# Kernel optimization log

Measured on AMD Instinct MI355X. Metric: run time of the kernel, lower is better.

The kernel has to match this reference:

```python
import jax, jax.numpy as jnp
import numpy as np

B, S, D = 4, 4096, 768

def setup_inputs() -> dict:
    key = jax.random.key(0)
    kx, kq, kk, kv = jax.random.split(key, 4)
    x = jax.random.normal(kx, (B, S, D), dtype=jnp.float32)
    Wq = jax.random.normal(kq, (D, D), dtype=jnp.float32) * (D ** -0.5)
    Wk = jax.random.normal(kk, (D, D), dtype=jnp.float32) * (D ** -0.5)
    Wv = jax.random.normal(kv, (D, D), dtype=jnp.float32) * (D ** -0.5)
    return {"x": x, "Wq": Wq, "Wk": Wk, "Wv": Wv}

def reference(x, Wq, Wk, Wv):
    # q,k,v: [B,S,D]  (Linear with no bias)
    q = x @ Wq
    k = x @ Wk
    v = x @ Wv
    # full N x N causal score matrix, as in the original module
    scores = jnp.einsum('bqd,bkd->bqk', q, k)  # [B,S,S]
    seq = scores.shape[1]
    causal_mask = jnp.triu(jnp.ones((seq, seq), dtype=bool), k=1)  # True above diagonal
    scores = jnp.where(causal_mask[None, :, :], -jnp.inf, scores)
    scale = jnp.asarray(k.shape[-1], scores.dtype) ** 0.5
    weights = jax.nn.softmax(scores / scale, axis=-1)  # [B,S,S]
    # dropout p=0.0 -> identity (deterministic reference)
    context = jnp.einsum('bqk,bkd->bqd', weights, v)  # [B,S,D]
    return context
```

## Files before the change

### kernel.cpp

```cpp
#include <hip/hip_runtime.h>
#include <hip/hip_bf16.h>

typedef __attribute__((ext_vector_type(8))) _Float16 half8_t;
typedef __attribute__((ext_vector_type(4))) _Float16 half4_t;
typedef __attribute__((ext_vector_type(4))) float float4_t;

#define D_DIM 768
#define S_DIM 4096
#define B_DIM 4
#define M_DIM (B_DIM * S_DIM)
#define SD ((size_t)S_DIM * D_DIM)

#define GLOAD_LDS16(g, s)                                      \
  __builtin_amdgcn_global_load_lds(                            \
      (const __attribute__((address_space(1))) void*)(g),      \
      (__attribute__((address_space(3))) void*)(s), 16, 0, 0)

__device__ __forceinline__ float4_t mfma16(half8_t a, half8_t b, float4_t c) {
  return __builtin_amdgcn_mfma_f32_16x16x32_f16(a, b, c, 0, 0, 0);
}

__global__ __launch_bounds__(256) void cvt_x_kernel(const float* __restrict__ in,
                                                    _Float16* __restrict__ out, int n) {
  int i = (blockIdx.x * 256 + threadIdx.x) * 4;
  if (i < n) {
    float4 v = *(const float4*)(in + i);
    half4_t o;
    o.x = (_Float16)v.x; o.y = (_Float16)v.y; o.z = (_Float16)v.z; o.w = (_Float16)v.w;
    *(half4_t*)(out + i) = o;
  }
}

__global__ __launch_bounds__(256) void transpose_w_kernel(const float* __restrict__ W0,
                                                          const float* __restrict__ W1,
                                                          const float* __restrict__ W2,
                                                          _Float16* __restrict__ WT) {
  const float* W = (blockIdx.z == 0) ? W0 : (blockIdx.z == 1) ? W1 : W2;
  _Float16* o = WT + (size_t)blockIdx.z * D_DIM * D_DIM;
  __shared__ _Float16 tile[64][68];
  int k0 = blockIdx.x * 64, n0 = blockIdx.y * 64;
#pragma unroll
  for (int i = 0; i < 16; ++i) {
    int idx = threadIdx.x + i * 256;
    int r = idx >> 6, c = idx & 63;
    tile[r][c] = (_Float16)W[(size_t)(k0 + r) * D_DIM + n0 + c];
  }
  __syncthreads();
#pragma unroll
  for (int i = 0; i < 16; ++i) {
    int idx = threadIdx.x + i * 256;
    int r = idx >> 6, c = idx & 63;
    o[(size_t)(n0 + r) * D_DIM + k0 + c] = tile[c][r];
  }
}

template <int NWC, int MF, int NF, int BN, bool SWAP>
__device__ __forceinline__ void gemm_core8(const _Float16* __restrict__ Ag,
                                           const _Float16* __restrict__ Bg,
                                           int lda, int ldb, int k0t, int nt,
                                           char* AshP, char* BshP,
                                           float4_t (&acc)[MF][NF]) {
  constexpr int BR = BN / 64;
  constexpr int ASZ = 256 * 128;
  constexpr int BSZ = BN * 128;
  const int tid = threadIdx.x;
  const int w = tid >> 6, l = tid & 63;
  const int wr = w / NWC, wc = w % NWC;
  const int l15 = l & 15, l4 = l >> 4;

  int sArow[4], sAu[4], sAdst[4];
#pragma unroll
  for (int i = 0; i < 4; ++i) {
    int L = i * 512 + tid;
    int row = L >> 3;
    sArow[i] = row;
    sAu[i] = ((L & 7) ^ (row & 7)) * 8;
    sAdst[i] = (i * 512 + (tid & ~63)) * 16;
  }
  int sBrow[BR], sBu[BR], sBdst[BR];
#pragma unroll
  for (int i = 0; i < BR; ++i) {
    int L = i * 512 + tid;
    int row = L >> 3;
    sBrow[i] = row;
    sBu[i] = ((L & 7) ^ (row & 7)) * 8;
    sBdst[i] = (i * 512 + (tid & ~63)) * 16;
  }

#define STAGE8(kt, s)                                                          \
  do {                                                                         \
    _Pragma("unroll") for (int i = 0; i < 4; ++i)                              \
        GLOAD_LDS16(Ag + (size_t)sArow[i] * lda + (kt)*64 + sAu[i],            \
                    AshP + (size_t)(s)*ASZ + sAdst[i]);                        \
    _Pragma("unroll") for (int i = 0; i < BR; ++i)                             \
        GLOAD_LDS16(Bg + (size_t)sBrow[i] * ldb + (kt)*64 + sBu[i],            \
                    BshP + (size_t)(s)*BSZ + sBdst[i]);                        \
  } while (0)

  STAGE8(k0t, 0);
  for (int t = 0; t < nt; ++t) {
    const int s = t & 1;
    const char* As = AshP + (size_t)s * ASZ;
    const char* Bs = BshP + (size_t)s * BSZ;
    asm volatile("s_waitcnt vmcnt(0)" ::: "memory");
    __builtin_amdgcn_s_barrier();
    __builtin_amdgcn_sched_barrier(0);
    if (t + 1 < nt) STAGE8(k0t + t + 1, s ^ 1);
    half8_t bf[NF][2];
#pragma unroll
    for (int ni = 0; ni < NF; ++ni) {
      int brow = wc * (NF * 16) + ni * 16 + l15;
      int bb = brow * 128 + ((l4 ^ (brow & 7)) * 16);
      bf[ni][0] = *(const half8_t*)(Bs + bb);
      bf[ni][1] = *(const half8_t*)(Bs + (bb ^ 64));
    }
    __builtin_amdgcn_s_setprio(1);
#pragma unroll
    for (int mq = 0; mq < MF / 4; ++mq) {
      half8_t af[4][2];
#pragma unroll
      for (int mi = 0; mi < 4; ++mi) {
        int arow = wr * (MF * 16) + (mq * 4 + mi) * 16 + l15;
        int ab = arow * 128 + ((l4 ^ (arow & 7)) * 16);
        af[mi][0] = *(const half8_t*)(As + ab);
        af[mi][1] = *(const half8_t*)(As + (ab ^ 64));
      }
#pragma unroll
      for (int mi = 0; mi < 4; ++mi)
#pragma unroll
        for (int ni = 0; ni < NF; ++ni) {
          if (SWAP) {
            acc[mq * 4 + mi][ni] = mfma16(bf[ni][0], af[mi][0], acc[mq * 4 + mi][ni]);
            acc[mq * 4 + mi][ni] = mfma16(bf[ni][1], af[mi][1], acc[mq * 4 + mi][ni]);
          } else {
            acc[mq * 4 + mi][ni] = mfma16(af[mi][0], bf[ni][0], acc[mq * 4 + mi][ni]);
            acc[mq * 4 + mi][ni] = mfma16(af[mi][1], bf[ni][1], acc[mq * 4 + mi][ni]);
          }
        }
    }
    __builtin_amdgcn_s_setprio(0);
  }
#undef STAGE8
}

__global__ __launch_bounds__(512, 2) void proj8_kernel(const _Float16* __restrict__ xh,
                                                       const _Float16* __restrict__ WT,
                                                       _Float16* __restrict__ qkv,
                                                       _Float16* __restrict__ vt) {
  __shared__ __align__(16) char Ash[2 * 256 * 128];
  __shared__ __align__(16) char Bsh[2 * 256 * 128];
  const int bid = blockIdx.x;
  const int wid = (bid & 7) * 72 + (bid >> 3);
  const int rg2 = wid / 18;
  const int rem = wid % 18;
  const int z = rem / 6;
  const int cb = (rem % 6) >> 1;
  const int rbg = rg2 * 2 + (rem & 1);

  const _Float16* Ag = xh + (size_t)rbg * 256 * D_DIM;
  const _Float16* Bg = WT + (size_t)z * D_DIM * D_DIM + (size_t)cb * 256 * D_DIM;
  float4_t acc[8][4];
#pragma unroll
  for (int a = 0; a < 8; ++a)
#pragma unroll
    for (int b = 0; b < 4; ++b) acc[a][b] = (float4_t){0.f, 0.f, 0.f, 0.f};

  const int tid = threadIdx.x;
  const int w = tid >> 6, l = tid & 63;
  const int wr = w >> 2, wc = w & 3;
  const int l15 = l & 15, l4 = l >> 4;

  if (z < 2) {
    gemm_core8<4, 8, 4, 256, false>(Ag, Bg, D_DIM, D_DIM, 0, 12, Ash, Bsh, acc);
    _Float16* C = qkv + (size_t)z * M_DIM * D_DIM;
#pragma unroll
    for (int mi = 0; mi < 8; ++mi)
#pragma unroll
      for (int ni = 0; ni < 4; ++ni) {
        int col = cb * 256 + wc * 64 + ni * 16 + l15;
#pragma unroll
        for (int j = 0; j < 4; ++j) {
          int row = rbg * 256 + wr * 128 + mi * 16 + l4 * 4 + j;
          C[(size_t)row * D_DIM + col] = (_Float16)acc[mi][ni][j];
        }
      }
  } else {
    gemm_core8<4, 8, 4, 256, true>(Ag, Bg, D_DIM, D_DIM, 0, 12, Ash, Bsh, acc);
#pragma unroll
    for (int mi = 0; mi < 8; ++mi) {
      int scol = rbg * 256 + wr * 128 + mi * 16 + l15;
      int bb = scol >> 12;
      int sl = scol & 4095;
      _Float16* vtb = vt + (size_t)bb * SD;
#pragma unroll
      for (int ni = 0; ni < 4; ++ni) {
#pragma unroll
        for (int j = 0; j < 4; ++j) {
          int drow = cb * 256 + wc * 64 + ni * 16 + l4 * 4 + j;
          vtb[(size_t)drow * S_DIM + sl] = (_Float16)acc[mi][ni][j];
        }
      }
    }
  }
}

__global__ __launch_bounds__(512, 2) void gemm1_8_kernel(const _Float16* __restrict__ Q,
                                                         const _Float16* __restrict__ K,
                                                         _Float16* __restrict__ P,
                                                         float* __restrict__ rp) {
  __shared__ __align__(16) char Ash[2 * 256 * 128];
  __shared__ __align__(16) char Bsh[2 * 256 * 128];
  const float SCALE = 0.036084391824351615f;
  const int bid = blockIdx.x;
  const int wid = (bid & 7) * 68 + (bid >> 3);
  const int z = wid / 136;
  const int t = wid % 136;
  int g, base;
  if (t < 10) { g = 0; base = 0; }
  else if (t < 36) { g = 1; base = 10; }
  else if (t < 78) { g = 2; base = 36; }
  else { g = 3; base = 78; }
  int r = t - base;
  int rbg, cb;
  if (r < 16 * g) {
    int cbg = r >> 4, wi = r & 15;
    rbg = 4 * g + (wi >> 2);
    cb = 4 * cbg + (wi & 3);
  } else {
    int r2 = r - 16 * g;
    const int ri[10] = {0, 1, 1, 2, 2, 2, 3, 3, 3, 3};
    const int rj[10] = {0, 0, 1, 0, 1, 2, 0, 1, 2, 3};
    rbg = 4 * g + ri[r2];
    cb = 4 * g + rj[r2];
  }

  const _Float16* Ag = Q + (size_t)z * SD + (size_t)rbg * 256 * D_DIM;
  const _Float16* Bg = K + (size_t)z * SD + (size_t)cb * 256 * D_DIM;
  float4_t acc[8][4];
#pragma unroll
  for (int a = 0; a < 8; ++a)
#pragma unroll
    for (int b = 0; b < 4; ++b) acc[a][b] = (float4_t){0.f, 0.f, 0.f, 0.f};
  gemm_core8<4, 8, 4, 256, false>(Ag, Bg, D_DIM, D_DIM, 0, 12, Ash, Bsh, acc);

  const int tid = threadIdx.x;
  const int w = tid >> 6, l = tid & 63;
  const int wr = w >> 2, wc = w & 3;
  const int l15 = l & 15, l4 = l >> 4;
  _Float16* Pz = P + (size_t)z * S_DIM * S_DIM;
  float* rpz = rp + (size_t)z * S_DIM * 64;
#pragma unroll
  for (int mi = 0; mi < 8; ++mi) {
#pragma unroll
    for (int j = 0; j < 4; ++j) {
      int row = rbg * 256 + wr * 128 + mi * 16 + l4 * 4 + j;
      float rs = 0.f;
#pragma unroll
      for (int ni = 0; ni < 4; ++ni) {
        int col = cb * 256 + wc * 64 + ni * 16 + l15;
        float v = (col <= row) ? __expf(acc[mi][ni][j] * SCALE - 4.0f) : 0.f;
        _Float16 ph = (_Float16)v;
        Pz[(size_t)row * S_DIM + col] = ph;
        rs += (float)ph;
      }
#pragma unroll
      for (int d = 1; d < 16; d <<= 1) rs += __shfl_xor(rs, d);
      if (l15 == 0) rpz[(size_t)row * 64 + cb * 4 + wc] = rs;
    }
  }
}

__global__ __launch_bounds__(256) void rsum_combine_kernel(const float* __restrict__ rp,
                                                           float* __restrict__ rsum) {
  int idx = blockIdx.x * 256 + threadIdx.x;
  int row = idx & 4095;
  int np = ((row >> 8) + 1) * 4;
  const float* p = rp + (size_t)idx * 64;
  float s = 0.f;
  for (int i = 0; i < np; ++i) s += p[i];
  rsum[idx] = s;
}

#define PART_STRIDE ((size_t)4 * 2048 * 768)
__global__ __launch_bounds__(512, 2) void gemm2_8_kernel(const _Float16* __restrict__ P,
                                                         const _Float16* __restrict__ VT,
                                                         float* __restrict__ outp,
                                                         _Float16* __restrict__ part,
                                                         const float* __restrict__ rsum) {
  __shared__ __align__(16) char Ash[2 * 256 * 128];
  __shared__ __align__(16) char Bsh[2 * 128 * 128];
  const int bid = blockIdx.x;
  const int wid = (bid & 7) * 72 + (bid >> 3);
  const int z = wid / 144;
  const int rem = wid % 144;
  const int job = rem / 6;
  const int by = rem % 6;
  int rbg, chunk;
  if (job < 16) { rbg = 15 - job; chunk = 0; } else { rbg = 31 - job; chunk = 1; }
  const int tot = 4 * (rbg + 1);
  const int k0t = chunk * 32;
  const int nt = (chunk == 0) ? (tot < 32 ? tot : 32) : (tot - 32);
  const bool split = (tot > 32);
  const _Float16* Ag = P + (size_t)z * S_DIM * S_DIM + (size_t)rbg * 256 * S_DIM;
  const _Float16* Bg = VT + (size_t)z * SD + (size_t)by * 128 * S_DIM;
  float4_t acc[4][4];
#pragma unroll
  for (int a = 0; a < 4; ++a)
#pragma unroll
    for (int b = 0; b < 4; ++b) acc[a][b] = (float4_t){0.f, 0.f, 0.f, 0.f};
  gemm_core8<2, 4, 4, 128, false>(Ag, Bg, S_DIM, S_DIM, k0t, nt, Ash, Bsh, acc);

  const int tid = threadIdx.x;
  const int w = tid >> 6, l = tid & 63;
  const int wr = w >> 1, wc = w & 1;
  const int l15 = l & 15, l4 = l >> 4;
#pragma unroll
  for (int mi = 0; mi < 4; ++mi) {
#pragma unroll
    for (int j = 0; j < 4; ++j) {
      int row = rbg * 256 + wr * 64 + mi * 16 + l4 * 4 + j;
      if (!split) {
        float rinv = 1.0f / rsum[(size_t)z * S_DIM + row];
#pragma unroll
        for (int ni = 0; ni < 4; ++ni) {
          int col = by * 128 + wc * 64 + ni * 16 + l15;
          outp[(size_t)z * SD + (size_t)row * D_DIM + col] = acc[mi][ni][j] * rinv;
        }
      } else {
        int lr = row - 2048;
#pragma unroll
        for (int ni = 0; ni < 4; ++ni) {
          int col = by * 128 + wc * 64 + ni * 16 + l15;
          part[(size_t)chunk * PART_STRIDE + ((size_t)z * 2048 + lr) * D_DIM + col] =
              (_Float16)acc[mi][ni][j];
        }
      }
    }
  }
}

__global__ __launch_bounds__(256) void g2_combine_kernel(const _Float16* __restrict__ part,
                                                         const float* __restrict__ rsum,
                                                         float* __restrict__ outp) {
  int idx = blockIdx.x * 256 + threadIdx.x;
  int z = idx / 196608;
  int rem = idx - z * 196608;
  int lr = rem / 96, c8 = rem - lr * 96;
  size_t off = ((size_t)z * 2048 + lr) * D_DIM + c8 * 8;
  half8_t p0 = *(const half8_t*)(part + off);
  half8_t p1 = *(const half8_t*)(part + PART_STRIDE + off);
  int row = 2048 + lr;
  float rinv = 1.0f / rsum[(size_t)z * S_DIM + row];
  float* o = outp + (size_t)z * SD + (size_t)row * D_DIM + c8 * 8;
#pragma unroll
  for (int e = 0; e < 8; ++e) o[e] = ((float)p0[e] + (float)p1[e]) * rinv;
}

extern "C" void kernel_launch(void* const* d_in, const int* in_sizes, int n_in,
                              void* d_out, int out_size, void* d_ws, size_t ws_size,
                              hipStream_t stream) {
  const float* x = (const float*)d_in[0];
  const float* Wq = (const float*)d_in[1];
  const float* Wk = (const float*)d_in[2];
  const float* Wv = (const float*)d_in[3];
  float* out = (float*)d_out;
  char* ws = (char*)d_ws;

  const size_t XH_B = (size_t)M_DIM * D_DIM * 2;
  const size_t QKV_B = 3 * XH_B;
  const size_t VT_B = XH_B;
  const size_t WT_B = (size_t)3 * D_DIM * D_DIM * 2;
  const size_t BASE_END = XH_B + QKV_B + VT_B + WT_B;

  _Float16* xh = (_Float16*)ws;
  _Float16* qkv = (_Float16*)(ws + XH_B);
  _Float16* Q = qkv;
  _Float16* K = qkv + (size_t)M_DIM * D_DIM;
  _Float16* vt = (_Float16*)(ws + XH_B + QKV_B);
  _Float16* wt = (_Float16*)(ws + XH_B + QKV_B + VT_B);

  float* rp = (float*)(ws + BASE_END);
  float* rsum = (float*)(ws + BASE_END + (size_t)4194304);
  _Float16* P = (_Float16*)(ws + BASE_END + (size_t)4259840);
  _Float16* part = xh;

  cvt_x_kernel<<<dim3(12288), dim3(256), 0, stream>>>(x, xh, M_DIM * D_DIM);
  transpose_w_kernel<<<dim3(12, 12, 3), dim3(256), 0, stream>>>(Wq, Wk, Wv, wt);
  proj8_kernel<<<dim3(576), dim3(512), 0, stream>>>(xh, wt, qkv, vt);
  gemm1_8_kernel<<<dim3(544), dim3(512), 0, stream>>>(Q, K, P, rp);
  rsum_combine_kernel<<<dim3(64), dim3(256), 0, stream>>>(rp, rsum);
  gemm2_8_kernel<<<dim3(576), dim3(512), 0, stream>>>(P, vt, out, part, rsum);
  g2_combine_kernel<<<dim3(3072), dim3(256), 0, stream>>>(part, rsum, out);
}
```

Baseline: 328.3 us.

## Replace double-buffered GEMM core with 4-stage K32 pipeline and 256x256 PV tiles

Replaces the shared GEMM core with a single 256x256 tile routine that stages K slices of 32 through a 4-slot LDS ring. Loads run three stages ahead, with partial vmcnt waits in place of a full drain each iteration. LDS grows to 128KB per block, so launch bounds drop to one block per CU. The PV GEMM moves from 256x128 tiles to 256x256 tiles with half as many blocks, and the XOR swizzle on LDS reads is removed, which may bring back bank conflicts.

```diff
diff --git a/kernel.cpp b/kernel.cpp
--- a/kernel.cpp
+++ b/kernel.cpp
@@ -54,101 +54,93 @@
   }
 }
 
-template <int NWC, int MF, int NF, int BN, bool SWAP>
-__device__ __forceinline__ void gemm_core8(const _Float16* __restrict__ Ag,
-                                           const _Float16* __restrict__ Bg,
-                                           int lda, int ldb, int k0t, int nt,
-                                           char* AshP, char* BshP,
-                                           float4_t (&acc)[MF][NF]) {
-  constexpr int BR = BN / 64;
-  constexpr int ASZ = 256 * 128;
-  constexpr int BSZ = BN * 128;
+template <bool SWAP>
+__device__ __forceinline__ void core256(const _Float16* __restrict__ Ag,
+                                        const _Float16* __restrict__ Bg,
+                                        int lda, int ldb, int k0, int nt,
+                                        char* lds, float4_t (&acc)[8][4]) {
   const int tid = threadIdx.x;
   const int w = tid >> 6, l = tid & 63;
-  const int wr = w / NWC, wc = w % NWC;
+  const int wr = w >> 2, wc = w & 3;
   const int l15 = l & 15, l4 = l >> 4;
 
-  int sArow[4], sAu[4], sAdst[4];
-#pragma unroll
-  for (int i = 0; i < 4; ++i) {
+  int aSrc[2], bSrc[2], sDst[2];
+#pragma unroll
+  for (int i = 0; i < 2; ++i) {
     int L = i * 512 + tid;
-    int row = L >> 3;
-    sArow[i] = row;
-    sAu[i] = ((L & 7) ^ (row & 7)) * 8;
-    sAdst[i] = (i * 512 + (tid & ~63)) * 16;
-  }
-  int sBrow[BR], sBu[BR], sBdst[BR];
-#pragma unroll
-  for (int i = 0; i < BR; ++i) {
-    int L = i * 512 + tid;
-    int row = L >> 3;
-    sBrow[i] = row;
-    sBu[i] = ((L & 7) ^ (row & 7)) * 8;
-    sBdst[i] = (i * 512 + (tid & ~63)) * 16;
-  }
-
-#define STAGE8(kt, s)                                                          \
-  do {                                                                         \
-    _Pragma("unroll") for (int i = 0; i < 4; ++i)                              \
-        GLOAD_LDS16(Ag + (size_t)sArow[i] * lda + (kt)*64 + sAu[i],            \
-                    AshP + (size_t)(s)*ASZ + sAdst[i]);                        \
-    _Pragma("unroll") for (int i = 0; i < BR; ++i)                             \
-        GLOAD_LDS16(Bg + (size_t)sBrow[i] * ldb + (kt)*64 + sBu[i],            \
-                    BshP + (size_t)(s)*BSZ + sBdst[i]);                        \
+    int row = L >> 2, u = L & 3;
+    aSrc[i] = row * lda + u * 8;
+    bSrc[i] = row * ldb + u * 8;
+    sDst[i] = (i * 512 + (tid & ~63)) * 16;
+  }
+
+#define STG(kt)                                                               \
+  do {                                                                        \
+    char* slot = lds + ((kt) & 3) * 32768;                                    \
+    const _Float16* Asrc = Ag + (size_t)(k0 + (kt)) * 32;                     \
+    const _Float16* Bsrc = Bg + (size_t)(k0 + (kt)) * 32;                     \
+    _Pragma("unroll") for (int i = 0; i < 2; ++i)                             \
+        GLOAD_LDS16(Asrc + aSrc[i], slot + sDst[i]);                          \
+    _Pragma("unroll") for (int i = 0; i < 2; ++i)                             \
+        GLOAD_LDS16(Bsrc + bSrc[i], slot + 16384 + sDst[i]);                  \
   } while (0)
 
-  STAGE8(k0t, 0);
-  for (int t = 0; t < nt; ++t) {
-    const int s = t & 1;
-    const char* As = AshP + (size_t)s * ASZ;
-    const char* Bs = BshP + (size_t)s * BSZ;
-    asm volatile("s_waitcnt vmcnt(0)" ::: "memory");
+#pragma unroll
+  for (int j = 0; j < 3; ++j)
+    if (j < nt) STG(j);
+
+#pragma unroll 1
+  for (int kt = 0; kt < nt; ++kt) {
+    __builtin_amdgcn_s_barrier();
+    if (kt + 3 < nt) STG(kt + 3);
+    __builtin_amdgcn_sched_barrier(0);
+    if (kt + 2 < nt)
+      asm volatile("s_waitcnt vmcnt(8)" ::: "memory");
+    else if (kt + 1 < nt)
+      asm volatile("s_waitcnt vmcnt(4)" ::: "memory");
+    else
+      asm volatile("s_waitcnt vmcnt(0)" ::: "memory");
+    __builtin_amdgcn_sched_barrier(0);
     __builtin_amdgcn_s_barrier();
     __builtin_amdgcn_sched_barrier(0);
-    if (t + 1 < nt) STAGE8(k0t + t + 1, s ^ 1);
-    half8_t bf[NF][2];
-#pragma unroll
-    for (int ni = 0; ni < NF; ++ni) {
-      int brow = wc * (NF * 16) + ni * 16 + l15;
-      int bb = brow * 128 + ((l4 ^ (brow & 7)) * 16);
-      bf[ni][0] = *(const half8_t*)(Bs + bb);
-      bf[ni][1] = *(const half8_t*)(Bs + (bb ^ 64));
+
+    const char* As = lds + (kt & 3) * 32768;
+    const char* Bs = As + 16384;
+    half8_t bf[4];
+#pragma unroll
+    for (int ni = 0; ni < 4; ++ni) {
+      int brow = wc * 64 + ni * 16 + l15;
+      bf[ni] = *(const half8_t*)(Bs + brow * 64 + l4 * 16);
     }
     __builtin_amdgcn_s_setprio(1);
 #pragma unroll
-    for (int mq = 0; mq < MF / 4; ++mq) {
-      half8_t af[4][2];
+    for (int mq = 0; mq < 2; ++mq) {
+      half8_t af[4];
 #pragma unroll
       for (int mi = 0; mi < 4; ++mi) {
-        int arow = wr * (MF * 16) + (mq * 4 + mi) * 16 + l15;
-        int ab = arow * 128 + ((l4 ^ (arow & 7)) * 16);
-        af[mi][0] = *(const half8_t*)(As + ab);
-        af[mi][1] = *(const half8_t*)(As + (ab ^ 64));
+        int arow = wr * 128 + (mq * 4 + mi) * 16 + l15;
+        af[mi] = *(const half8_t*)(As + arow * 64 + l4 * 16);
       }
 #pragma unroll
       for (int mi = 0; mi < 4; ++mi)
 #pragma unroll
-        for (int ni = 0; ni < NF; ++ni) {
-          if (SWAP) {
-            acc[mq * 4 + mi][ni] = mfma16(bf[ni][0], af[mi][0], acc[mq * 4 + mi][ni]);
-            acc[mq * 4 + mi][ni] = mfma16(bf[ni][1], af[mi][1], acc[mq * 4 + mi][ni]);
-          } else {
-            acc[mq * 4 + mi][ni] = mfma16(af[mi][0], bf[ni][0], acc[mq * 4 + mi][ni]);
-            acc[mq * 4 + mi][ni] = mfma16(af[mi][1], bf[ni][1], acc[mq * 4 + mi][ni]);
-          }
+        for (int ni = 0; ni < 4; ++ni) {
+          if (SWAP)
+            acc[mq * 4 + mi][ni] = mfma16(bf[ni], af[mi], acc[mq * 4 + mi][ni]);
+          else
+            acc[mq * 4 + mi][ni] = mfma16(af[mi], bf[ni], acc[mq * 4 + mi][ni]);
         }
     }
     __builtin_amdgcn_s_setprio(0);
   }
-#undef STAGE8
-}
-
-__global__ __launch_bounds__(512, 2) void proj8_kernel(const _Float16* __restrict__ xh,
+#undef STG
+}
+
+__global__ __launch_bounds__(512, 1) void proj8_kernel(const _Float16* __restrict__ xh,
                                                        const _Float16* __restrict__ WT,
                                                        _Float16* __restrict__ qkv,
                                                        _Float16* __restrict__ vt) {
-  __shared__ __align__(16) char Ash[2 * 256 * 128];
-  __shared__ __align__(16) char Bsh[2 * 256 * 128];
+  __shared__ __align__(16) char lds[131072];
   const int bid = blockIdx.x;
   const int wid = (bid & 7) * 72 + (bid >> 3);
   const int rg2 = wid / 18;
@@ -171,7 +163,7 @@
   const int l15 = l & 15, l4 = l >> 4;
 
   if (z < 2) {
-    gemm_core8<4, 8, 4, 256, false>(Ag, Bg, D_DIM, D_DIM, 0, 12, Ash, Bsh, acc);
+    core256<false>(Ag, Bg, D_DIM, D_DIM, 0, 24, lds, acc);
     _Float16* C = qkv + (size_t)z * M_DIM * D_DIM;
 #pragma unroll
     for (int mi = 0; mi < 8; ++mi)
@@ -185,7 +177,7 @@
         }
       }
   } else {
-    gemm_core8<4, 8, 4, 256, true>(Ag, Bg, D_DIM, D_DIM, 0, 12, Ash, Bsh, acc);
+    core256<true>(Ag, Bg, D_DIM, D_DIM, 0, 24, lds, acc);
 #pragma unroll
     for (int mi = 0; mi < 8; ++mi) {
       int scol = rbg * 256 + wr * 128 + mi * 16 + l15;
@@ -204,12 +196,11 @@
   }
 }
 
-__global__ __launch_bounds__(512, 2) void gemm1_8_kernel(const _Float16* __restrict__ Q,
+__global__ __launch_bounds__(512, 1) void gemm1_8_kernel(const _Float16* __restrict__ Q,
                                                          const _Float16* __restrict__ K,
                                                          _Float16* __restrict__ P,
                                                          float* __restrict__ rp) {
-  __shared__ __align__(16) char Ash[2 * 256 * 128];
-  __shared__ __align__(16) char Bsh[2 * 256 * 128];
+  __shared__ __align__(16) char lds[131072];
   const float SCALE = 0.036084391824351615f;
   const int bid = blockIdx.x;
   const int wid = (bid & 7) * 68 + (bid >> 3);
@@ -241,7 +232,7 @@
   for (int a = 0; a < 8; ++a)
 #pragma unroll
     for (int b = 0; b < 4; ++b) acc[a][b] = (float4_t){0.f, 0.f, 0.f, 0.f};
-  gemm_core8<4, 8, 4, 256, false>(Ag, Bg, D_DIM, D_DIM, 0, 12, Ash, Bsh, acc);
+  core256<false>(Ag, Bg, D_DIM, D_DIM, 0, 24, lds, acc);
 
   const int tid = threadIdx.x;
   const int w = tid >> 6, l = tid & 63;
@@ -282,55 +273,54 @@
 }
 
 #define PART_STRIDE ((size_t)4 * 2048 * 768)
-__global__ __launch_bounds__(512, 2) void gemm2_8_kernel(const _Float16* __restrict__ P,
+__global__ __launch_bounds__(512, 1) void gemm2_8_kernel(const _Float16* __restrict__ P,
                                                          const _Float16* __restrict__ VT,
                                                          float* __restrict__ outp,
                                                          _Float16* __restrict__ part,
                                                          const float* __restrict__ rsum) {
-  __shared__ __align__(16) char Ash[2 * 256 * 128];
-  __shared__ __align__(16) char Bsh[2 * 128 * 128];
+  __shared__ __align__(16) char lds[131072];
   const int bid = blockIdx.x;
-  const int wid = (bid & 7) * 72 + (bid >> 3);
-  const int z = wid / 144;
-  const int rem = wid % 144;
-  const int job = rem / 6;
-  const int by = rem % 6;
+  const int wid = (bid & 7) * 36 + (bid >> 3);
+  const int z = wid / 72;
+  const int rem = wid % 72;
+  const int job = rem / 3;
+  const int by = rem % 3;
   int rbg, chunk;
   if (job < 16) { rbg = 15 - job; chunk = 0; } else { rbg = 31 - job; chunk = 1; }
-  const int tot = 4 * (rbg + 1);
-  const int k0t = chunk * 32;
-  const int nt = (chunk == 0) ? (tot < 32 ? tot : 32) : (tot - 32);
-  const bool split = (tot > 32);
+  const int tot = 8 * (rbg + 1);
+  const int k0 = chunk * 64;
+  const int nt = (chunk == 0) ? (tot < 64 ? tot : 64) : (tot - 64);
+  const bool split = (tot > 64);
   const _Float16* Ag = P + (size_t)z * S_DIM * S_DIM + (size_t)rbg * 256 * S_DIM;
-  const _Float16* Bg = VT + (size_t)z * SD + (size_t)by * 128 * S_DIM;
-  float4_t acc[4][4];
-#pragma unroll
-  for (int a = 0; a < 4; ++a)
+  const _Float16* Bg = VT + (size_t)z * SD + (size_t)by * 256 * S_DIM;
+  float4_t acc[8][4];
+#pragma unroll
+  for (int a = 0; a < 8; ++a)
 #pragma unroll
     for (int b = 0; b < 4; ++b) acc[a][b] = (float4_t){0.f, 0.f, 0.f, 0.f};
-  gemm_core8<2, 4, 4, 128, false>(Ag, Bg, S_DIM, S_DIM, k0t, nt, Ash, Bsh, acc);
+  core256<false>(Ag, Bg, S_DIM, S_DIM, k0, nt, lds, acc);
 
   const int tid = threadIdx.x;
   const int w = tid >> 6, l = tid & 63;
-  const int wr = w >> 1, wc = w & 1;
+  const int wr = w >> 2, wc = w & 3;
   const int l15 = l & 15, l4 = l >> 4;
 #pragma unroll
-  for (int mi = 0; mi < 4; ++mi) {
+  for (int mi = 0; mi < 8; ++mi) {
 #pragma unroll
     for (int j = 0; j < 4; ++j) {
-      int row = rbg * 256 + wr * 64 + mi * 16 + l4 * 4 + j;
+      int row = rbg * 256 + wr * 128 + mi * 16 + l4 * 4 + j;
       if (!split) {
         float rinv = 1.0f / rsum[(size_t)z * S_DIM + row];
 #pragma unroll
         for (int ni = 0; ni < 4; ++ni) {
-          int col = by * 128 + wc * 64 + ni * 16 + l15;
+          int col = by * 256 + wc * 64 + ni * 16 + l15;
           outp[(size_t)z * SD + (size_t)row * D_DIM + col] = acc[mi][ni][j] * rinv;
         }
       } else {
         int lr = row - 2048;
 #pragma unroll
         for (int ni = 0; ni < 4; ++ni) {
-          int col = by * 128 + wc * 64 + ni * 16 + l15;
+          int col = by * 256 + wc * 64 + ni * 16 + l15;
           part[(size_t)chunk * PART_STRIDE + ((size_t)z * 2048 + lr) * D_DIM + col] =
               (_Float16)acc[mi][ni][j];
         }
@@ -389,6 +379,6 @@
   proj8_kernel<<<dim3(576), dim3(512), 0, stream>>>(xh, wt, qkv, vt);
   gemm1_8_kernel<<<dim3(544), dim3(512), 0, stream>>>(Q, K, P, rp);
   rsum_combine_kernel<<<dim3(64), dim3(256), 0, stream>>>(rp, rsum);
-  gemm2_8_kernel<<<dim3(576), dim3(512), 0, stream>>>(P, vt, out, part, rsum);
+  gemm2_8_kernel<<<dim3(288), dim3(512), 0, stream>>>(P, vt, out, part, rsum);
   g2_combine_kernel<<<dim3(3072), dim3(256), 0, stream>>>(part, rsum, out);
 }
```

Result: slower. 344.0 us (+4.8%).
